# Kernel optimization log

Hardware: AMD Instinct MI355X
Metric: run time of the kernel (lower is better)

## Reference

```python
import jax, jax.numpy as jnp
import numpy as np

TEMP_LEN = 16
TARGET_LEN = 22
DIM = 768
HEADS = 12
B = 16
NT = TEMP_LEN * TEMP_LEN          # 256 template tokens
NG = TARGET_LEN * TARGET_LEN      # 484 target tokens
N = NT + NG                       # 740
POS_HID = 512


def _gaussian_heatmap(center, size, sig=1.0):
    x_axis = np.linspace(0, size[0] - 1, size[0]) - center[0]
    y_axis = np.linspace(0, size[1] - 1, size[1]) - center[1]
    xx, yy = np.meshgrid(x_axis, y_axis)
    return np.exp(-0.5 * (xx ** 2 + yy ** 2) / sig ** 2)


def _bias_index(L):
    # faithful to getBiasIndex (w_len == h_len here)
    coords = np.stack(np.meshgrid(np.arange(L), np.arange(L), indexing='ij'))  # [2,L,L]
    flat = coords.reshape(2, -1)                                               # [2,L*L]
    rel = (flat[:, :, None] - flat[:, None, :]).transpose(1, 2, 0).astype(np.int64)
    rel[:, :, 0] += L - 1
    rel[:, :, 1] += L - 1
    rel[:, :, 0] *= 2 * L - 1
    return rel.sum(-1)  # [L*L, L*L]


def setup_inputs() -> dict:
    key = jax.random.key(0)
    ks = jax.random.split(key, 12)
    f32 = jnp.float32
    x = jax.random.normal(ks[0], (B, N, DIM), dtype=f32)
    temp_q = jax.random.normal(ks[1], (B, NT, DIM), dtype=f32)
    target_q = jax.random.normal(ks[2], (B, NG, DIM), dtype=f32)
    # linear weights stored [in, out] (transposed torch layout)
    w = lambda k, i, o: jax.random.normal(k, (i, o), dtype=f32) * 0.02
    q_w = w(ks[3], DIM, DIM)
    k_w = w(ks[4], DIM, DIM)
    v_w = w(ks[5], DIM, DIM)
    proj_w = w(ks[6], DIM, DIM)
    proj_b = jnp.zeros((DIM,), dtype=f32)
    rpb_table = jax.random.normal(ks[7], ((2 * TARGET_LEN - 1) ** 2, HEADS), dtype=f32) * 0.0002
    rpb_table_temp = jax.random.normal(ks[8], ((2 * TEMP_LEN - 1) ** 2, HEADS), dtype=f32) * 0.0002
    pos_w1 = w(ks[9], 2, POS_HID)
    pos_b1 = jnp.zeros((POS_HID,), dtype=f32)
    pos_w2 = w(ks[10], POS_HID, HEADS)
    pos_b2 = jnp.zeros((HEADS,), dtype=f32)
    # deterministic cross-bias coordinate table (non-learned buffer)
    temp_tab = _gaussian_heatmap((TEMP_LEN // 2, TEMP_LEN // 2), (TEMP_LEN, TEMP_LEN)).astype(np.float32).flatten() \
        + np.linspace(-0.2, 0.2, NT, dtype=np.float32)
    targ_tab = _gaussian_heatmap((TARGET_LEN // 2, TARGET_LEN // 2), (TARGET_LEN, TARGET_LEN)).astype(np.float32).flatten() \
        + np.linspace(-0.2, 0.2, NG, dtype=np.float32)
    # torch.meshgrid default indexing='ij': [2, NT, NG] -> permute(1,2,0) -> [NT,NG,2]
    temp_target = np.stack(np.meshgrid(temp_tab, targ_tab, indexing='ij')).transpose(1, 2, 0)
    target_temp_tab = jnp.asarray(temp_target.transpose(1, 0, 2))  # [NG, NT, 2]
    temp_idx = jnp.asarray(_bias_index(TEMP_LEN))       # [NT, NT] int64
    target_idx = jnp.asarray(_bias_index(TARGET_LEN))   # [NG, NG] int64
    return {
        'x': x, 'temp_q': temp_q, 'target_q': target_q,
        'q_w': q_w, 'k_w': k_w, 'v_w': v_w, 'proj_w': proj_w, 'proj_b': proj_b,
        'rpb_table': rpb_table, 'rpb_table_temp': rpb_table_temp,
        'pos_w1': pos_w1, 'pos_b1': pos_b1, 'pos_w2': pos_w2, 'pos_b2': pos_b2,
        'target_temp_tab': target_temp_tab,
        'temp_idx': temp_idx, 'target_idx': target_idx,
    }


def reference(x, temp_q, target_q, q_w, k_w, v_w, proj_w, proj_b,
              rpb_table, rpb_table_temp, pos_w1, pos_b1, pos_w2, pos_b2,
              target_temp_tab, temp_idx, target_idx):
    Bsz, Ntok, C = x.shape
    H = HEADS
    hd = C // H
    scale = hd ** -0.5

    q_in = jnp.concatenate([temp_q, target_q], axis=1)                 # [B,N,C]
    q = (q_in @ q_w).reshape(Bsz, Ntok, H, hd).transpose(0, 2, 1, 3)   # [B,H,N,hd]
    k = (x @ k_w).reshape(Bsz, Ntok, H, hd).transpose(0, 2, 1, 3)
    v = (x @ v_w).reshape(Bsz, Ntok, H, hd).transpose(0, 2, 1, 3)

    # gathered relative position biases -> [H, Ni, Ni]
    temp_rpb = rpb_table_temp[temp_idx.reshape(-1)].reshape(NT, NT, H).transpose(2, 0, 1)
    targ_rpb = rpb_table[target_idx.reshape(-1)].reshape(NG, NG, H).transpose(2, 0, 1)
    # MLP cross bias: [NG, NT, 2] -> [NG, NT, H] -> [H, NG, NT]
    hid = jax.nn.relu(target_temp_tab @ pos_w1 + pos_b1)
    target_temp_bias = (hid @ pos_w2 + pos_b2).transpose(2, 0, 1)      # [H,NG,NT]
    temp_target_bias = target_temp_bias.transpose(0, 2, 1)             # [H,NT,NG]
    top = jnp.concatenate([temp_rpb, temp_target_bias], axis=2)        # [H,NT,N]
    bot = jnp.concatenate([target_temp_bias, targ_rpb], axis=2)        # [H,NG,N]
    bias = jnp.concatenate([top, bot], axis=1)[None]                   # [1,H,N,N]

    attn = jnp.einsum('bhnd,bhmd->bhnm', q, k) * scale + bias
    attn = jax.nn.softmax(attn, axis=-1)
    out = jnp.einsum('bhnm,bhmd->bhnd', attn, v).transpose(0, 2, 1, 3).reshape(Bsz, Ntok, C)
    return out @ proj_w + proj_b
```

## Files before the change

kernel.cpp:

```cpp
#include <hip/hip_runtime.h>


typedef unsigned short u16;
typedef short bf16x8 __attribute__((ext_vector_type(8)));
typedef float f32x4 __attribute__((ext_vector_type(4)));

#define BSZ   16
#define NTOK  740
#define NTMP  256
#define NTGT  484
#define DIMC  768
#define NHEAD 12
#define HDIM  64
#define MROWS (BSZ*NTOK)
#define SMAX  16.0f

__device__ __forceinline__ float bf2f(u16 u) {
    return __uint_as_float(((unsigned int)u) << 16);
}
__device__ __forceinline__ float bflo(unsigned int u) {
    return __uint_as_float(u << 16);
}
__device__ __forceinline__ float bfhi(unsigned int u) {
    return __uint_as_float(u & 0xffff0000u);
}
__device__ __forceinline__ u16 f2bf(float f) {
    unsigned int u = __float_as_uint(f);
    u += 0x7fffu + ((u >> 16) & 1u);
    return (u16)(u >> 16);
}

__device__ __forceinline__ void gl_lds16(const u16* g, u16* l) {
    __builtin_amdgcn_global_load_lds(
        (const __attribute__((address_space(1))) unsigned int*)(unsigned long long)g,
        (__attribute__((address_space(3))) unsigned int*)(unsigned int)(unsigned long long)l,
        16, 0, 0);
}

__device__ __forceinline__ size_t b2off(int h, int i, int j) {
    return ((size_t)(h * NTOK + i)) * 768 + ((j >> 6) << 6) + ((j & 15) << 2) + ((j >> 4) & 3);
}

#define PREP_MLP  484
#define PREP_CONV (PREP_MLP + 2220)
#define PREP_TRW  (PREP_CONV + 576)
#define PREP_ALL  (PREP_TRW + 2220)

__global__ __launch_bounds__(256) void prep_kernel(
    const float* __restrict__ x, const float* __restrict__ tq,
    const float* __restrict__ gq, u16* __restrict__ XB, u16* __restrict__ QB,
    const float* __restrict__ w0, const float* __restrict__ w1,
    const float* __restrict__ w2, const float* __restrict__ w3,
    u16* __restrict__ Wt,
    const float* __restrict__ rpb, const float* __restrict__ rpbt,
    const int* __restrict__ tidx, const int* __restrict__ gidx,
    const float* __restrict__ pw1, const float* __restrict__ pb1,
    const float* __restrict__ pw2, const float* __restrict__ pb2,
    const float* __restrict__ tab, u16* __restrict__ bias)
{
    __shared__ float T[64][65];
    const int blk = blockIdx.x;
    const int tid = threadIdx.x;

    if (blk < PREP_MLP) {
        int g = blk;
        int t = tid;
        float a  = tab[(g * NTMP + t) * 2 + 0];
        float bb = tab[(g * NTMP + t) * 2 + 1];
        float acc[NHEAD];
        #pragma unroll
        for (int h = 0; h < NHEAD; h++) acc[h] = pb2[h];
        for (int k = 0; k < 512; k++) {
            float hid = fmaxf(a * pw1[k] + bb * pw1[512 + k] + pb1[k], 0.0f);
            #pragma unroll
            for (int h = 0; h < NHEAD; h++) acc[h] += hid * pw2[k * NHEAD + h];
        }
        #pragma unroll
        for (int h = 0; h < NHEAD; h++) {
            u16 v = f2bf(acc[h]);
            bias[b2off(h, t, NTMP + g)] = v;
            bias[b2off(h, NTMP + g, t)] = v;
        }
    } else if (blk < PREP_CONV) {
        int t0 = (blk - PREP_MLP) * 512 + tid;
        int t1 = t0 + 256;
        const float* xs0 = x + (size_t)t0 * 8;
        const float* xs1 = x + (size_t)t1 * 8;
        float4 xa0 = ((const float4*)xs0)[0], xa1 = ((const float4*)xs0)[1];
        float4 xb0 = ((const float4*)xs1)[0], xb1 = ((const float4*)xs1)[1];
        int r0 = t0 / 96, cc0 = (t0 - r0 * 96) * 8;
        int b0 = r0 / NTOK, n0 = r0 - b0 * NTOK;
        const float* qs0 = (n0 < NTMP)
                         ? tq + ((size_t)(b0 * NTMP + n0)) * DIMC + cc0
                         : gq + ((size_t)(b0 * NTGT + (n0 - NTMP))) * DIMC + cc0;
        int r1 = t1 / 96, cc1 = (t1 - r1 * 96) * 8;
        int b1 = r1 / NTOK, n1 = r1 - b1 * NTOK;
        const float* qs1 = (n1 < NTMP)
                         ? tq + ((size_t)(b1 * NTMP + n1)) * DIMC + cc1
                         : gq + ((size_t)(b1 * NTGT + (n1 - NTMP))) * DIMC + cc1;
        float4 qa0 = ((const float4*)qs0)[0], qa1 = ((const float4*)qs0)[1];
        float4 qb0 = ((const float4*)qs1)[0], qb1 = ((const float4*)qs1)[1];
        {
            u16 e[8] = {f2bf(xa0.x), f2bf(xa0.y), f2bf(xa0.z), f2bf(xa0.w),
                        f2bf(xa1.x), f2bf(xa1.y), f2bf(xa1.z), f2bf(xa1.w)};
            *(uint4*)(XB + (size_t)t0 * 8) = *(uint4*)e;
        }
        {
            u16 e[8] = {f2bf(xb0.x), f2bf(xb0.y), f2bf(xb0.z), f2bf(xb0.w),
                        f2bf(xb1.x), f2bf(xb1.y), f2bf(xb1.z), f2bf(xb1.w)};
            *(uint4*)(XB + (size_t)t1 * 8) = *(uint4*)e;
        }
        {
            u16 e[8] = {f2bf(qa0.x), f2bf(qa0.y), f2bf(qa0.z), f2bf(qa0.w),
                        f2bf(qa1.x), f2bf(qa1.y), f2bf(qa1.z), f2bf(qa1.w)};
            *(uint4*)(QB + (size_t)r0 * DIMC + cc0) = *(uint4*)e;
        }
        {
            u16 e[8] = {f2bf(qb0.x), f2bf(qb0.y), f2bf(qb0.z), f2bf(qb0.w),
                        f2bf(qb1.x), f2bf(qb1.y), f2bf(qb1.z), f2bf(qb1.w)};
            *(uint4*)(QB + (size_t)r1 * DIMC + cc1) = *(uint4*)e;
        }
    } else if (blk < PREP_TRW) {
        int t = blk - PREP_CONV;
        int z = t / 144, rem = t - z * 144;
        int bx = rem % 12, by = rem / 12;
        const float* src = (z == 0) ? w0 : (z == 1) ? w1 : (z == 2) ? w2 : w3;
        const float scale = (z == 0) ? 0.125f : 1.0f;
        u16* dst = Wt + (size_t)z * DIMC * DIMC;
        int out0 = bx * 64, in0 = by * 64;
        #pragma unroll
        for (int l = 0; l < 4; l++) {
            int u = tid + (l << 8);
            int r = u >> 4, c4 = (u & 15) << 2;
            float4 p = *(const float4*)(src + (size_t)(in0 + r) * DIMC + out0 + c4);
            T[r][c4] = p.x; T[r][c4 + 1] = p.y; T[r][c4 + 2] = p.z; T[r][c4 + 3] = p.w;
        }
        __syncthreads();
        #pragma unroll
        for (int l = 0; l < 2; l++) {
            int u = tid + (l << 8);
            int r = u >> 3, c8 = (u & 7) << 3;
            u16 e[8];
            #pragma unroll
            for (int i = 0; i < 8; i++) e[i] = f2bf(T[c8 + i][r] * scale);
            *(uint4*)(dst + (size_t)(out0 + r) * DIMC + in0 + c8) = *(uint4*)e;
        }
    } else {
        int t = blk - PREP_TRW;
        int jb = t % 3, i = t / 3;
        int j = jb * 256 + tid;
        u16 vals[NHEAD];
        if (j >= NTOK) {
            u16 neg = f2bf(-1e30f);
            #pragma unroll
            for (int h = 0; h < NHEAD; h++) vals[h] = neg;
        } else if (i < NTMP && j < NTMP) {
            int idx = tidx[i * NTMP + j];
            #pragma unroll
            for (int h = 0; h < NHEAD; h++) vals[h] = f2bf(rpbt[idx * NHEAD + h]);
        } else if (i >= NTMP && j >= NTMP) {
            int idx = gidx[(i - NTMP) * NTGT + (j - NTMP)];
            #pragma unroll
            for (int h = 0; h < NHEAD; h++) vals[h] = f2bf(rpb[idx * NHEAD + h]);
        } else {
            return;
        }
        #pragma unroll
        for (int h = 0; h < NHEAD; h++) bias[b2off(h, i, j)] = vals[h];
    }
}

template<int MODE>
__global__ __launch_bounds__(256) void gemm_bf16(
    const u16* __restrict__ A, const u16* __restrict__ Wt,
    const float* __restrict__ pb, u16* __restrict__ C0,
    u16* __restrict__ C1, float* __restrict__ Cf)
{
    __shared__ __align__(16) u16 As[2][8192];
    __shared__ __align__(16) u16 Bs[2][8192];
    const int tid = threadIdx.x;
    const int lane = tid & 63, w = tid >> 6;
    const int quad = lane >> 4, ln = lane & 15;

    const int gx = gridDim.x;
    const int nwg = gx * (int)gridDim.y;
    const int flat = blockIdx.y * gx + blockIdx.x;
    const int q = nwg >> 3, r = nwg & 7;
    const int xcd = flat & 7, sidx = flat >> 3;
    const int wg = (xcd < r) ? xcd * (q + 1) + sidx
                             : r * (q + 1) + (xcd - r) * q + sidx;
    const int by = wg / gx, bx = wg - by * gx;

    const int m0 = by << 7;
    const int wm = (w >> 1) << 6, wn = (w & 1) << 6;

    const int nn = bx << 7;
    const u16* Wbase = Wt + (size_t)nn * DIMC;
    u16* Cb;
    int col0;
    if (MODE == 1) {
        if (nn < DIMC) { col0 = nn; Cb = C0; }
        else           { col0 = nn - DIMC; Cb = C1; }
    } else {
        col0 = nn; Cb = C0;
    }

    f32x4 acc[4][4];
    #pragma unroll
    for (int i = 0; i < 4; i++)
        #pragma unroll
        for (int j = 0; j < 4; j++)
            acc[i][j] = (f32x4){0.f, 0.f, 0.f, 0.f};

#define STAGE(s, k0) do {                                                     \
    _Pragma("unroll")                                                         \
    for (int l = 0; l < 4; l++) {                                             \
        int f = tid + (l << 8);                                  \
        int c8 = f >> 7, rr = f & 127;                                        \
        int grow = m0 + rr; if (grow >= MROWS) grow = MROWS - 1;              \
        gl_lds16(A + (size_t)grow * DIMC + (k0) + c8 * 8, &As[s][f * 8]);     \
        gl_lds16(Wbase + (size_t)rr * DIMC + (k0) + c8 * 8, &Bs[s][f * 8]);   \
    } } while (0)

#define COMPUTE(s) do {                                                       \
    _Pragma("unroll")                                                         \
    for (int kp = 0; kp < 2; kp++) {                                          \
        bf16x8 af[4], bfr[4];                                                 \
        _Pragma("unroll")                                                     \
        for (int mt = 0; mt < 4; mt++)                                        \
            af[mt] = *(const bf16x8*)                                         \
                &As[s][(((kp << 2) + quad) * 128 + wm + mt * 16 + ln) * 8];   \
        _Pragma("unroll")                                                     \
        for (int nt = 0; nt < 4; nt++)                                        \
            bfr[nt] = *(const bf16x8*)                                        \
                &Bs[s][(((kp << 2) + quad) * 128 + wn + nt * 16 + ln) * 8];   \
        _Pragma("unroll")                                                     \
        for (int mt = 0; mt < 4; mt++)                                        \
            _Pragma("unroll")                                                 \
            for (int nt = 0; nt < 4; nt++)                                    \
                acc[mt][nt] = __builtin_amdgcn_mfma_f32_16x16x32_bf16(        \
                    af[mt], bfr[nt], acc[mt][nt], 0, 0, 0);                   \
    } } while (0)

    STAGE(0, 0);
    __syncthreads();
    #pragma unroll 1
    for (int t = 0; t < 12; t += 2) {
        STAGE(1, (t + 1) << 6);
        COMPUTE(0);
        __syncthreads();
        if (t < 10) STAGE(0, (t + 2) << 6);
        COMPUTE(1);
        __syncthreads();
    }

#undef STAGE
#undef COMPUTE

    #pragma unroll
    for (int mt = 0; mt < 4; mt++) {
        #pragma unroll
        for (int reg = 0; reg < 4; reg++) {
            int grow = m0 + wm + mt * 16 + (quad << 2) + reg;
            if (grow >= MROWS) continue;
            #pragma unroll
            for (int nt = 0; nt < 4; nt++) {
                int gcol = col0 + wn + nt * 16 + ln;
                float v = acc[mt][nt][reg];
                if (MODE == 2) {
                    Cf[(size_t)grow * DIMC + gcol] = v + pb[gcol];
                } else {
                    Cb[(size_t)grow * DIMC + gcol] = f2bf(v);
                }
            }
        }
    }
}

__global__ __launch_bounds__(256) void attn_mfma(
    const u16* __restrict__ Qg, const u16* __restrict__ Kg,
    const u16* __restrict__ Vg, const u16* __restrict__ bias,
    u16* __restrict__ ctx)
{
    __shared__ __align__(16) u16 KsL[4096];
    __shared__ __align__(16) u16 VtL[64 * 72];
    __shared__ __align__(16) u16 Pw[4][16][72];

    const int tid = threadIdx.x;
    const int lane = tid & 63, w = tid >> 6;
    const int quad = lane >> 4, ln = lane & 15;

    const int flat = (blockIdx.z * 12 + blockIdx.y) * 12 + blockIdx.x;
    const int wg = (flat & 7) * 288 + (flat >> 3);
    const int h = wg / 192;
    const int rem = wg - h * 192;
    const int b = rem / 12;
    const int q0 = (rem - b * 12) << 6;

    const int mbase = q0 + (w << 4);
    const u16* bp = bias + ((size_t)h * NTOK) * 768;

    bf16x8 aq[2];
    {
        int qrow = mbase + ln; if (qrow >= NTOK) qrow = NTOK - 1;
        #pragma unroll
        for (int kp = 0; kp < 2; kp++)
            aq[kp] = *(const bf16x8*)(Qg + ((size_t)(b * NTOK + qrow)) * DIMC
                                      + h * HDIM + kp * 32 + (quad << 3));
    }
    int boff[4];
    #pragma unroll
    for (int reg = 0; reg < 4; reg++) {
        int rr = mbase + (quad << 2) + reg;
        if (rr >= NTOK) rr = NTOK - 1;
        boff[reg] = rr * 768 + (ln << 2);
    }

    const int pswz = ((ln >> 2) & 3) << 4;

    float rs[4] = {};
    f32x4 O[4];
    #pragma unroll
    for (int dt = 0; dt < 4; dt++) O[dt] = (f32x4){0.f, 0.f, 0.f, 0.f};

    for (int j0 = 0; j0 < NTOK; j0 += 64) {
        __syncthreads();
        #pragma unroll
        for (int l = 0; l < 2; l++) {
            int f = tid + (l << 8);
            int chunk = f >> 6, jr = f & 63;
            int krow = j0 + jr; if (krow >= NTOK) krow = NTOK - 1;
            gl_lds16(Kg + ((size_t)(b * NTOK + krow)) * DIMC + h * HDIM + chunk * 8,
                     KsL + f * 8);
        }
        uint2 bvv[4];
        #pragma unroll
        for (int reg = 0; reg < 4; reg++)
            bvv[reg] = *(const uint2*)(bp + boff[reg] + j0);
        #pragma unroll
        for (int l = 0; l < 2; l++) {
            int u = tid + (l << 8);
            int jr = u >> 3, d0 = (u & 7) << 3;
            int vrow = j0 + jr; if (vrow >= NTOK) vrow = NTOK - 1;
            uint4 p = *(const uint4*)(Vg + ((size_t)(b * NTOK + vrow)) * DIMC + h * HDIM + d0);
            const u16* pe = (const u16*)&p;
            int jswz = jr ^ d0;
            #pragma unroll
            for (int i = 0; i < 8; i++) VtL[(d0 + i) * 72 + jswz] = pe[i];
        }
        __syncthreads();

        bf16x8 bv[4][2];
        #pragma unroll
        for (int dt = 0; dt < 4; dt++) {
            int key8 = ((dt * 2 + (ln >> 3)) & 7) << 3;
            #pragma unroll
            for (int kp = 0; kp < 2; kp++) {
                int koff = (kp * 32 + (quad << 3)) ^ key8;
                bv[dt][kp] = *(const bf16x8*)&VtL[(dt * 16 + ln) * 72 + koff];
            }
        }

        f32x4 s[4];
        #pragma unroll
        for (int nt = 0; nt < 4; nt++) s[nt] = (f32x4){0.f, 0.f, 0.f, 0.f};
        __builtin_amdgcn_s_setprio(1);
        #pragma unroll
        for (int kp = 0; kp < 2; kp++)
            #pragma unroll
            for (int nt = 0; nt < 4; nt++) {
                bf16x8 bk = *(const bf16x8*)
                    &KsL[(((kp << 2) + quad) * 64 + nt * 16 + ln) * 8];
                s[nt] = __builtin_amdgcn_mfma_f32_16x16x32_bf16(aq[kp], bk, s[nt], 0, 0, 0);
            }
        __builtin_amdgcn_s_setprio(0);

        #pragma unroll
        for (int reg = 0; reg < 4; reg++) {
            uint2 bb = bvv[reg];
            float p0 = __expf(s[0][reg] + bflo(bb.x) - SMAX);
            float p1 = __expf(s[1][reg] + bfhi(bb.x) - SMAX);
            float p2 = __expf(s[2][reg] + bflo(bb.y) - SMAX);
            float p3 = __expf(s[3][reg] + bfhi(bb.y) - SMAX);
            s[0][reg] = p0; s[1][reg] = p1;
            s[2][reg] = p2; s[3][reg] = p3;
            rs[reg] += p0 + p1 + p2 + p3;
        }
        u16* pwb = &Pw[w][0][0];
        #pragma unroll
        for (int nt = 0; nt < 4; nt++) {
            int colw = ((nt ^ quad) << 4) + ln;
            #pragma unroll
            for (int reg = 0; reg < 4; reg++)
                pwb[((quad << 2) + reg) * 72 + colw] = f2bf(s[nt][reg]);
        }
        bf16x8 ap[2];
        #pragma unroll
        for (int kp = 0; kp < 2; kp++) {
            int koff = (kp * 32 + (quad << 3)) ^ pswz;
            ap[kp] = *(const bf16x8*)&pwb[ln * 72 + koff];
        }
        __builtin_amdgcn_s_setprio(1);
        #pragma unroll
        for (int dt = 0; dt < 4; dt++)
            #pragma unroll
            for (int kp = 0; kp < 2; kp++)
                O[dt] = __builtin_amdgcn_mfma_f32_16x16x32_bf16(
                    ap[kp], bv[dt][kp], O[dt], 0, 0, 0);
        __builtin_amdgcn_s_setprio(0);
    }

    #pragma unroll
    for (int reg = 0; reg < 4; reg++) {
        float t = rs[reg];
        #pragma unroll
        for (int mk = 8; mk >= 1; mk >>= 1) t += __shfl_xor(t, mk);
        float inv = 1.0f / t;
        int row = mbase + (quad << 2) + reg;
        if (row < NTOK) {
            #pragma unroll
            for (int dt = 0; dt < 4; dt++)
                ctx[((size_t)(b * NTOK + row)) * DIMC + h * HDIM + dt * 16 + ln]
                    = f2bf(O[dt][reg] * inv);
        }
    }
}

extern "C" void kernel_launch(void* const* d_in, const int* in_sizes, int n_in,
                              void* d_out, int out_size, void* d_ws, size_t ws_size,
                              hipStream_t stream)
{
    const float* x        = (const float*)d_in[0];
    const float* temp_q   = (const float*)d_in[1];
    const float* target_q = (const float*)d_in[2];
    const float* q_w      = (const float*)d_in[3];
    const float* k_w      = (const float*)d_in[4];
    const float* v_w      = (const float*)d_in[5];
    const float* proj_w   = (const float*)d_in[6];
    const float* proj_b   = (const float*)d_in[7];
    const float* rpb      = (const float*)d_in[8];
    const float* rpbt     = (const float*)d_in[9];
    const float* pw1      = (const float*)d_in[10];
    const float* pb1      = (const float*)d_in[11];
    const float* pw2      = (const float*)d_in[12];
    const float* pb2      = (const float*)d_in[13];
    const float* tab      = (const float*)d_in[14];
    const int*   tidx     = (const int*)d_in[15];
    const int*   gidx     = (const int*)d_in[16];
    float* out = (float*)d_out;

    char* ws = (char*)d_ws;
    const size_t S = (size_t)MROWS * DIMC * sizeof(u16);
    const size_t SZB = (size_t)NHEAD * NTOK * 768 * sizeof(u16);
    u16* XB    = (u16*)(ws);
    u16* QB    = (u16*)(ws + S);
    u16* Q     = (u16*)(ws + 2 * S);
    u16* K     = (u16*)(ws + 3 * S);
    u16* V     = QB;
    u16* CTX   = XB;
    u16* BIAS2 = (u16*)(ws + 4 * S);
    u16* WT    = (u16*)(ws + 4 * S + SZB);

    prep_kernel<<<dim3(PREP_ALL), 256, 0, stream>>>(
        x, temp_q, target_q, XB, QB,
        q_w, k_w, v_w, proj_w, WT,
        rpb, rpbt, tidx, gidx,
        pw1, pb1, pw2, pb2, tab, BIAS2);

    const u16* WTq = WT;
    const u16* WTk = WT + (size_t)DIMC * DIMC;
    const u16* WTp = WT + 3 * (size_t)DIMC * DIMC;

    gemm_bf16<0><<<dim3(6, 93), 256, 0, stream>>>(QB, WTq, nullptr, Q, nullptr, nullptr);
    gemm_bf16<1><<<dim3(12, 93), 256, 0, stream>>>(XB, WTk, nullptr, K, V, nullptr);
    attn_mfma<<<dim3(12, 12, 16), 256, 0, stream>>>(Q, K, V, BIAS2, CTX);
    gemm_bf16<2><<<dim3(6, 93), 256, 0, stream>>>(CTX, WTp, proj_b, nullptr, nullptr, out);
}
```

Measured before the change: 452.3 us.

## Fold log2e into Q weights and biases, use exp2, packed bf16 convert, single-buffer Q GEMM

```diff
diff --git a/kernel.cpp b/kernel.cpp
--- a/kernel.cpp
+++ b/kernel.cpp
@@ -13,11 +13,9 @@
 #define NHEAD 12
 #define HDIM  64
 #define MROWS (BSZ*NTOK)
-#define SMAX  16.0f
-
-__device__ __forceinline__ float bf2f(u16 u) {
-    return __uint_as_float(((unsigned int)u) << 16);
-}
+#define LOG2E 1.44269504f
+#define NEGS  (-23.0831032f)
+
 __device__ __forceinline__ float bflo(unsigned int u) {
     return __uint_as_float(u << 16);
 }
@@ -77,7 +75,7 @@
         }
         #pragma unroll
         for (int h = 0; h < NHEAD; h++) {
-            u16 v = f2bf(acc[h]);
+            u16 v = f2bf(acc[h] * LOG2E);
             bias[b2off(h, t, NTMP + g)] = v;
             bias[b2off(h, NTMP + g, t)] = v;
         }
@@ -125,7 +123,7 @@
         int z = t / 144, rem = t - z * 144;
         int bx = rem % 12, by = rem / 12;
         const float* src = (z == 0) ? w0 : (z == 1) ? w1 : (z == 2) ? w2 : w3;
-        const float scale = (z == 0) ? 0.125f : 1.0f;
+        const float scale = (z == 0) ? 0.125f * LOG2E : 1.0f;
         u16* dst = Wt + (size_t)z * DIMC * DIMC;
         int out0 = bx * 64, in0 = by * 64;
         #pragma unroll
@@ -157,11 +155,11 @@
         } else if (i < NTMP && j < NTMP) {
             int idx = tidx[i * NTMP + j];
             #pragma unroll
-            for (int h = 0; h < NHEAD; h++) vals[h] = f2bf(rpbt[idx * NHEAD + h]);
+            for (int h = 0; h < NHEAD; h++) vals[h] = f2bf(rpbt[idx * NHEAD + h] * LOG2E);
         } else if (i >= NTMP && j >= NTMP) {
             int idx = gidx[(i - NTMP) * NTGT + (j - NTMP)];
             #pragma unroll
-            for (int h = 0; h < NHEAD; h++) vals[h] = f2bf(rpb[idx * NHEAD + h]);
+            for (int h = 0; h < NHEAD; h++) vals[h] = f2bf(rpb[idx * NHEAD + h] * LOG2E);
         } else {
             return;
         }
@@ -170,14 +168,14 @@
     }
 }
 
-template<int MODE>
+template<int MODE, bool DB>
 __global__ __launch_bounds__(256) void gemm_bf16(
     const u16* __restrict__ A, const u16* __restrict__ Wt,
     const float* __restrict__ pb, u16* __restrict__ C0,
     u16* __restrict__ C1, float* __restrict__ Cf)
 {
-    __shared__ __align__(16) u16 As[2][8192];
-    __shared__ __align__(16) u16 Bs[2][8192];
+    __shared__ __align__(16) u16 As[DB ? 2 : 1][8192];
+    __shared__ __align__(16) u16 Bs[DB ? 2 : 1][8192];
     const int tid = threadIdx.x;
     const int lane = tid & 63, w = tid >> 6;
     const int quad = lane >> 4, ln = lane & 15;
@@ -242,16 +240,26 @@
                     af[mt], bfr[nt], acc[mt][nt], 0, 0, 0);                   \
     } } while (0)
 
-    STAGE(0, 0);
-    __syncthreads();
-    #pragma unroll 1
-    for (int t = 0; t < 12; t += 2) {
-        STAGE(1, (t + 1) << 6);
-        COMPUTE(0);
+    if constexpr (DB) {
+        STAGE(0, 0);
         __syncthreads();
-        if (t < 10) STAGE(0, (t + 2) << 6);
-        COMPUTE(1);
-        __syncthreads();
+        #pragma unroll 1
+        for (int t = 0; t < 12; t += 2) {
+            STAGE(1, (t + 1) << 6);
+            COMPUTE(0);
+            __syncthreads();
+            if (t < 10) STAGE(0, (t + 2) << 6);
+            COMPUTE(1);
+            __syncthreads();
+        }
+    } else {
+        #pragma unroll 1
+        for (int t = 0; t < 12; t++) {
+            __syncthreads();
+            STAGE(0, t << 6);
+            __syncthreads();
+            COMPUTE(0);
+        }
     }
 
 #undef STAGE
@@ -317,6 +325,10 @@
     }
 
     const int pswz = ((ln >> 2) & 3) << 4;
+    const int c0 = ((0 ^ quad) << 4) + ln;
+    const int c1 = ((1 ^ quad) << 4) + ln;
+    const int c2 = ((2 ^ quad) << 4) + ln;
+    const int c3 = ((3 ^ quad) << 4) + ln;
 
     float rs[4] = {};
     f32x4 O[4];
@@ -363,7 +375,7 @@
 
         f32x4 s[4];
         #pragma unroll
-        for (int nt = 0; nt < 4; nt++) s[nt] = (f32x4){0.f, 0.f, 0.f, 0.f};
+        for (int nt = 0; nt < 4; nt++) s[nt] = (f32x4){NEGS, NEGS, NEGS, NEGS};
         __builtin_amdgcn_s_setprio(1);
         #pragma unroll
         for (int kp = 0; kp < 2; kp++)
@@ -378,21 +390,27 @@
         #pragma unroll
         for (int reg = 0; reg < 4; reg++) {
             uint2 bb = bvv[reg];
-            float p0 = __expf(s[0][reg] + bflo(bb.x) - SMAX);
-            float p1 = __expf(s[1][reg] + bfhi(bb.x) - SMAX);
-            float p2 = __expf(s[2][reg] + bflo(bb.y) - SMAX);
-            float p3 = __expf(s[3][reg] + bfhi(bb.y) - SMAX);
+            float p0 = __builtin_exp2f(s[0][reg] + bflo(bb.x));
+            float p1 = __builtin_exp2f(s[1][reg] + bfhi(bb.x));
+            float p2 = __builtin_exp2f(s[2][reg] + bflo(bb.y));
+            float p3 = __builtin_exp2f(s[3][reg] + bfhi(bb.y));
             s[0][reg] = p0; s[1][reg] = p1;
             s[2][reg] = p2; s[3][reg] = p3;
             rs[reg] += p0 + p1 + p2 + p3;
         }
         u16* pwb = &Pw[w][0][0];
         #pragma unroll
-        for (int nt = 0; nt < 4; nt++) {
-            int colw = ((nt ^ quad) << 4) + ln;
-            #pragma unroll
-            for (int reg = 0; reg < 4; reg++)
-                pwb[((quad << 2) + reg) * 72 + colw] = f2bf(s[nt][reg]);
+        for (int reg = 0; reg < 4; reg++) {
+            int ro = ((quad << 2) + reg) * 72;
+            unsigned int r01, r23;
+            asm("v_cvt_pk_bf16_f32 %0, %1, %2"
+                : "=v"(r01) : "v"(s[0][reg]), "v"(s[1][reg]));
+            asm("v_cvt_pk_bf16_f32 %0, %1, %2"
+                : "=v"(r23) : "v"(s[2][reg]), "v"(s[3][reg]));
+            pwb[ro + c0] = (u16)r01;
+            pwb[ro + c1] = (u16)(r01 >> 16);
+            pwb[ro + c2] = (u16)r23;
+            pwb[ro + c3] = (u16)(r23 >> 16);
         }
         bf16x8 ap[2];
         #pragma unroll
@@ -471,8 +489,8 @@
     const u16* WTk = WT + (size_t)DIMC * DIMC;
     const u16* WTp = WT + 3 * (size_t)DIMC * DIMC;
 
-    gemm_bf16<0><<<dim3(6, 93), 256, 0, stream>>>(QB, WTq, nullptr, Q, nullptr, nullptr);
-    gemm_bf16<1><<<dim3(12, 93), 256, 0, stream>>>(XB, WTk, nullptr, K, V, nullptr);
+    gemm_bf16<0, false><<<dim3(6, 93), 256, 0, stream>>>(QB, WTq, nullptr, Q, nullptr, nullptr);
+    gemm_bf16<1, true ><<<dim3(12, 93), 256, 0, stream>>>(XB, WTk, nullptr, K, V, nullptr);
     attn_mfma<<<dim3(12, 12, 16), 256, 0, stream>>>(Q, K, V, BIAS2, CTX);
-    gemm_bf16<2><<<dim3(6, 93), 256, 0, stream>>>(CTX, WTp, proj_b, nullptr, nullptr, out);
-}
+    gemm_bf16<2, true ><<<dim3(6, 93), 256, 0, stream>>>(CTX, WTp, proj_b, nullptr, nullptr, out);
+}
```

New measurement: 452.5 us. About the same (+0.0%).

## Use exp2 softmax with log2e-folded scales and 64-row single-buffered GEMM tiles

Applied to the files above, without the earlier changes.

```diff
diff --git a/kernel.cpp b/kernel.cpp
--- a/kernel.cpp
+++ b/kernel.cpp
@@ -13,11 +13,9 @@
 #define NHEAD 12
 #define HDIM  64
 #define MROWS (BSZ*NTOK)
-#define SMAX  16.0f
-
-__device__ __forceinline__ float bf2f(u16 u) {
-    return __uint_as_float(((unsigned int)u) << 16);
-}
+#define LOG2E 1.44269504f
+#define NEGS  (-23.0831032f)
+
 __device__ __forceinline__ float bflo(unsigned int u) {
     return __uint_as_float(u << 16);
 }
@@ -77,7 +75,7 @@
         }
         #pragma unroll
         for (int h = 0; h < NHEAD; h++) {
-            u16 v = f2bf(acc[h]);
+            u16 v = f2bf(acc[h] * LOG2E);
             bias[b2off(h, t, NTMP + g)] = v;
             bias[b2off(h, NTMP + g, t)] = v;
         }
@@ -125,7 +123,7 @@
         int z = t / 144, rem = t - z * 144;
         int bx = rem % 12, by = rem / 12;
         const float* src = (z == 0) ? w0 : (z == 1) ? w1 : (z == 2) ? w2 : w3;
-        const float scale = (z == 0) ? 0.125f : 1.0f;
+        const float scale = (z == 0) ? 0.125f * LOG2E : 1.0f;
         u16* dst = Wt + (size_t)z * DIMC * DIMC;
         int out0 = bx * 64, in0 = by * 64;
         #pragma unroll
@@ -157,16 +155,16 @@
         } else if (i < NTMP && j < NTMP) {
             int idx = tidx[i * NTMP + j];
             #pragma unroll
-            for (int h = 0; h < NHEAD; h++) vals[h] = f2bf(rpbt[idx * NHEAD + h]);
+            for (int h = 0; h < NHEAD; h++) vals[h] = f2bf(rpbt[idx * NHEAD + h] * LOG2E);
         } else if (i >= NTMP && j >= NTMP) {
             int idx = gidx[(i - NTMP) * NTGT + (j - NTMP)];
             #pragma unroll
-            for (int h = 0; h < NHEAD; h++) vals[h] = f2bf(rpb[idx * NHEAD + h]);
+            for (int h = 0; h < NHEAD; h++) vals[h] = f2bf(rpb[idx * NHEAD + h] * LOG2E);
         } else {
             return;
         }
         #pragma unroll
-        for (int h = 0; h < NHEAD; h++) bias[b2off(h, i, j)] = vals[h];
+        for (int h = 0; h < NHEAD; h++) vals[h], bias[b2off(h, i, j)] = vals[h];
     }
 }
 
@@ -176,8 +174,8 @@
     const float* __restrict__ pb, u16* __restrict__ C0,
     u16* __restrict__ C1, float* __restrict__ Cf)
 {
-    __shared__ __align__(16) u16 As[2][8192];
-    __shared__ __align__(16) u16 Bs[2][8192];
+    __shared__ __align__(16) u16 As[4096];
+    __shared__ __align__(16) u16 Bs[8192];
     const int tid = threadIdx.x;
     const int lane = tid & 63, w = tid >> 6;
     const int quad = lane >> 4, ln = lane & 15;
@@ -191,8 +189,8 @@
                              : r * (q + 1) + (xcd - r) * q + sidx;
     const int by = wg / gx, bx = wg - by * gx;
 
-    const int m0 = by << 7;
-    const int wm = (w >> 1) << 6, wn = (w & 1) << 6;
+    const int m0 = by << 6;
+    const int wm = (w >> 1) << 5, wn = (w & 1) << 6;
 
     const int nn = bx << 7;
     const u16* Wbase = Wt + (size_t)nn * DIMC;
@@ -205,64 +203,55 @@
         col0 = nn; Cb = C0;
     }
 
-    f32x4 acc[4][4];
+    f32x4 acc[2][4];
     #pragma unroll
-    for (int i = 0; i < 4; i++)
+    for (int i = 0; i < 2; i++)
         #pragma unroll
         for (int j = 0; j < 4; j++)
             acc[i][j] = (f32x4){0.f, 0.f, 0.f, 0.f};
 
-#define STAGE(s, k0) do {                                                     \
-    _Pragma("unroll")                                                         \
-    for (int l = 0; l < 4; l++) {                                             \
-        int f = tid + (l << 8);                                  \
-        int c8 = f >> 7, rr = f & 127;                                        \
-        int grow = m0 + rr; if (grow >= MROWS) grow = MROWS - 1;              \
-        gl_lds16(A + (size_t)grow * DIMC + (k0) + c8 * 8, &As[s][f * 8]);     \
-        gl_lds16(Wbase + (size_t)rr * DIMC + (k0) + c8 * 8, &Bs[s][f * 8]);   \
-    } } while (0)
-
-#define COMPUTE(s) do {                                                       \
-    _Pragma("unroll")                                                         \
-    for (int kp = 0; kp < 2; kp++) {                                          \
-        bf16x8 af[4], bfr[4];                                                 \
-        _Pragma("unroll")                                                     \
-        for (int mt = 0; mt < 4; mt++)                                        \
-            af[mt] = *(const bf16x8*)                                         \
-                &As[s][(((kp << 2) + quad) * 128 + wm + mt * 16 + ln) * 8];   \
-        _Pragma("unroll")                                                     \
-        for (int nt = 0; nt < 4; nt++)                                        \
-            bfr[nt] = *(const bf16x8*)                                        \
-                &Bs[s][(((kp << 2) + quad) * 128 + wn + nt * 16 + ln) * 8];   \
-        _Pragma("unroll")                                                     \
-        for (int mt = 0; mt < 4; mt++)                                        \
-            _Pragma("unroll")                                                 \
-            for (int nt = 0; nt < 4; nt++)                                    \
-                acc[mt][nt] = __builtin_amdgcn_mfma_f32_16x16x32_bf16(        \
-                    af[mt], bfr[nt], acc[mt][nt], 0, 0, 0);                   \
-    } } while (0)
-
-    STAGE(0, 0);
-    __syncthreads();
     #pragma unroll 1
-    for (int t = 0; t < 12; t += 2) {
-        STAGE(1, (t + 1) << 6);
-        COMPUTE(0);
+    for (int t = 0; t < 12; t++) {
         __syncthreads();
-        if (t < 10) STAGE(0, (t + 2) << 6);
-        COMPUTE(1);
+        const int k0 = t << 6;
+        #pragma unroll
+        for (int l = 0; l < 2; l++) {
+            int f = tid + (l << 8);
+            int c8 = f >> 6, rr = f & 63;
+            gl_lds16(A + (size_t)(m0 + rr) * DIMC + k0 + c8 * 8, &As[f * 8]);
+        }
+        #pragma unroll
+        for (int l = 0; l < 4; l++) {
+            int f = tid + (l << 8);
+            int c8 = f >> 7, rr = f & 127;
+            gl_lds16(Wbase + (size_t)rr * DIMC + k0 + c8 * 8, &Bs[f * 8]);
+        }
         __syncthreads();
-    }
-
-#undef STAGE
-#undef COMPUTE
+        #pragma unroll
+        for (int kp = 0; kp < 2; kp++) {
+            bf16x8 af[2], bfr[4];
+            #pragma unroll
+            for (int mt = 0; mt < 2; mt++)
+                af[mt] = *(const bf16x8*)
+                    &As[(((kp << 2) + quad) * 64 + wm + mt * 16 + ln) * 8];
+            #pragma unroll
+            for (int nt = 0; nt < 4; nt++)
+                bfr[nt] = *(const bf16x8*)
+                    &Bs[(((kp << 2) + quad) * 128 + wn + nt * 16 + ln) * 8];
+            #pragma unroll
+            for (int mt = 0; mt < 2; mt++)
+                #pragma unroll
+                for (int nt = 0; nt < 4; nt++)
+                    acc[mt][nt] = __builtin_amdgcn_mfma_f32_16x16x32_bf16(
+                        af[mt], bfr[nt], acc[mt][nt], 0, 0, 0);
+        }
+    }
 
     #pragma unroll
-    for (int mt = 0; mt < 4; mt++) {
+    for (int mt = 0; mt < 2; mt++) {
         #pragma unroll
         for (int reg = 0; reg < 4; reg++) {
             int grow = m0 + wm + mt * 16 + (quad << 2) + reg;
-            if (grow >= MROWS) continue;
             #pragma unroll
             for (int nt = 0; nt < 4; nt++) {
                 int gcol = col0 + wn + nt * 16 + ln;
@@ -363,7 +352,7 @@
 
         f32x4 s[4];
         #pragma unroll
-        for (int nt = 0; nt < 4; nt++) s[nt] = (f32x4){0.f, 0.f, 0.f, 0.f};
+        for (int nt = 0; nt < 4; nt++) s[nt] = (f32x4){NEGS, NEGS, NEGS, NEGS};
         __builtin_amdgcn_s_setprio(1);
         #pragma unroll
         for (int kp = 0; kp < 2; kp++)
@@ -378,10 +367,10 @@
         #pragma unroll
         for (int reg = 0; reg < 4; reg++) {
             uint2 bb = bvv[reg];
-            float p0 = __expf(s[0][reg] + bflo(bb.x) - SMAX);
-            float p1 = __expf(s[1][reg] + bfhi(bb.x) - SMAX);
-            float p2 = __expf(s[2][reg] + bflo(bb.y) - SMAX);
-            float p3 = __expf(s[3][reg] + bfhi(bb.y) - SMAX);
+            float p0 = __builtin_exp2f(s[0][reg] + bflo(bb.x));
+            float p1 = __builtin_exp2f(s[1][reg] + bfhi(bb.x));
+            float p2 = __builtin_exp2f(s[2][reg] + bflo(bb.y));
+            float p3 = __builtin_exp2f(s[3][reg] + bfhi(bb.y));
             s[0][reg] = p0; s[1][reg] = p1;
             s[2][reg] = p2; s[3][reg] = p3;
             rs[reg] += p0 + p1 + p2 + p3;
@@ -471,8 +460,8 @@
     const u16* WTk = WT + (size_t)DIMC * DIMC;
     const u16* WTp = WT + 3 * (size_t)DIMC * DIMC;
 
-    gemm_bf16<0><<<dim3(6, 93), 256, 0, stream>>>(QB, WTq, nullptr, Q, nullptr, nullptr);
-    gemm_bf16<1><<<dim3(12, 93), 256, 0, stream>>>(XB, WTk, nullptr, K, V, nullptr);
+    gemm_bf16<0><<<dim3(6, 185), 256, 0, stream>>>(QB, WTq, nullptr, Q, nullptr, nullptr);
+    gemm_bf16<1><<<dim3(12, 185), 256, 0, stream>>>(XB, WTk, nullptr, K, V, nullptr);
     attn_mfma<<<dim3(12, 12, 16), 256, 0, stream>>>(Q, K, V, BIAS2, CTX);
-    gemm_bf16<2><<<dim3(6, 93), 256, 0, stream>>>(CTX, WTp, proj_b, nullptr, nullptr, out);
-}
+    gemm_bf16<2><<<dim3(6, 185), 256, 0, stream>>>(CTX, WTp, proj_b, nullptr, nullptr, out);
+}
```

New measurement: 456.1 us. No clear change (+0.8%).
